# Performance work log

Measured on AMD Instinct MI355X. Metric: run time of the kernel, lower is better.

## Reference

```python
import jax, jax.numpy as jnp
import numpy as np

NUM_HEADS = 16
HEAD_DIM = 64
SCALE = HEAD_DIM ** (-0.5)


def setup_inputs() -> dict:
    key = jax.random.key(0)
    ks = jax.random.split(key, 7)
    B, T, S, D = 8, 1024, 1500, 1024
    std = 1.0 / np.sqrt(D)
    return {
        "x": jax.random.normal(ks[0], (B, T, D), jnp.float32),
        "k": jax.random.normal(ks[1], (B, S, D), jnp.float32),
        "v": jax.random.normal(ks[2], (B, S, D), jnp.float32),
        "wq": jax.random.normal(ks[3], (D, D), jnp.float32) * std,
        "bq": jnp.zeros((D,), jnp.float32),
        "wo": jax.random.normal(ks[4], (D, D), jnp.float32) * std,
        "bo": jnp.zeros((D,), jnp.float32),
    }


def reference(x, k, v, wq, bq, wo, bo):
    B, T, D = x.shape
    H, Dh = NUM_HEADS, HEAD_DIM
    # q_proj (torch Linear: x @ W^T + b), pre-scaled
    q = (jnp.einsum("btd,ed->bte", x, wq) + bq) * SCALE
    q = q.reshape(B, T, H, Dh)                      # bthd
    kh = k.reshape(B, -1, H, Dh)                    # bshd
    vh = v.reshape(B, -1, H, Dh)
    scores = jnp.einsum("bthd,bshd->bhts", q, kh)   # full [B,H,T,S]
    probs = jax.nn.softmax(scores, axis=-1)
    out = jnp.einsum("bhts,bshd->bthd", probs, vh).reshape(B, T, D)
    return jnp.einsum("btd,ed->bte", out, wo) + bo
```

## Files before the change

kernel.cpp:

```cpp
#include <hip/hip_runtime.h>
#include <hip/hip_bf16.h>

typedef __attribute__((ext_vector_type(8))) short short8;
typedef __attribute__((ext_vector_type(4))) float floatx4;

#define B_ 8
#define T_ 1024
#define S_ 1500
#define SP 1536
#define D_ 1024
#define H_ 16
#define DH 64
#define SCALE2_ 0.1803368801111244f

__device__ __forceinline__ unsigned short f2bf(float f) {
  unsigned u = __float_as_uint(f);
  u += 0x7fffu + ((u >> 16) & 1u);
  return (unsigned short)(u >> 16);
}

__device__ __forceinline__ floatx4 mfma16(short8 a, short8 b, floatx4 c) {
  return __builtin_amdgcn_mfma_f32_16x16x32_bf16(a, b, c, 0, 0, 0);
}

__device__ __forceinline__ void gload_lds16(const unsigned short* g, unsigned short* l) {
  __builtin_amdgcn_global_load_lds(
      (const __attribute__((address_space(1))) unsigned int*)g,
      (__attribute__((address_space(3))) unsigned int*)(unsigned long)(uintptr_t)l, 16, 0, 0);
}

#define N1C (B_ * T_ * D_ / 4)
#define N2C (D_ * D_ / 4)
#define NB_CAST ((N1C + 2 * N2C) / 256)
#define NB_PK (B_ * H_ * SP * 16 / 256)
#define NB_PVT ((SP / 64) * B_ * H_)
__global__ void prep_kernel(const float* __restrict__ x, const float* __restrict__ k,
                            const float* __restrict__ v, const float* __restrict__ wq,
                            const float* __restrict__ wo,
                            unsigned short* __restrict__ xb,
                            unsigned short* __restrict__ wqb,
                            unsigned short* __restrict__ wob,
                            unsigned short* __restrict__ kb,
                            unsigned short* __restrict__ vt) {
  __shared__ unsigned short tile[64][72];
  int bid = blockIdx.x;
  int t = threadIdx.x;
  if (bid < NB_CAST) {
    int i = bid * 256 + t;
    const float* src;
    unsigned short* dst;
    int j;
    if (i < N1C) {
      src = x; dst = xb; j = i;
    } else if (i < N1C + N2C) {
      src = wq; dst = wqb; j = i - N1C;
    } else {
      src = wo; dst = wob; j = i - N1C - N2C;
    }
    float4 val = ((const float4*)src)[j];
    ushort4 o;
    o.x = f2bf(val.x); o.y = f2bf(val.y); o.z = f2bf(val.z); o.w = f2bf(val.w);
    ((ushort4*)dst)[j] = o;
  } else if (bid < NB_CAST + NB_PK) {
    int i = (bid - NB_CAST) * 256 + t;
    int dh4 = (i & 15) * 4;
    int j = i >> 4;
    int s = j % SP;
    int bh = j / SP;
    if (bh < B_ * H_) {
      int b = bh >> 4, h = bh & 15;
      int p = s & 31;
      int src = (s & ~31) + ((p >> 2) & 3) * 8 + ((p >> 4) & 1) * 4 + (p & 3);
      ushort4 o;
      if (src < S_) {
        float4 val = *(const float4*)(k + (((size_t)(b * S_ + src) * H_ + h) * DH) + dh4);
        o.x = f2bf(val.x); o.y = f2bf(val.y); o.z = f2bf(val.z); o.w = f2bf(val.w);
      } else {
        o = make_ushort4(0, 0, 0, 0);
      }
      *(ushort4*)(kb + ((size_t)bh * SP + s) * DH + dh4) = o;
    }
  } else {
    int q = bid - NB_CAST - NB_PK;
    int st = q % (SP / 64), bh = q / (SP / 64);
    int b = bh >> 4, h = bh & 15;
    int s0 = st * 64;
    for (int i = t; i < 1024; i += 256) {
      int sl = i >> 4, dh4 = (i & 15) * 4;
      float4 val = make_float4(0.f, 0.f, 0.f, 0.f);
      if (s0 + sl < S_)
        val = *(const float4*)(v + ((size_t)((b * S_ + s0 + sl) * H_ + h)) * DH + dh4);
      tile[dh4 + 0][sl] = f2bf(val.x);
      tile[dh4 + 1][sl] = f2bf(val.y);
      tile[dh4 + 2][sl] = f2bf(val.z);
      tile[dh4 + 3][sl] = f2bf(val.w);
    }
    __syncthreads();
    for (int i = t; i < 1024; i += 256) {
      int d = i >> 4, s4 = (i & 15) * 4;
      ushort4 o;
      o.x = tile[d][s4]; o.y = tile[d][s4 + 1]; o.z = tile[d][s4 + 2]; o.w = tile[d][s4 + 3];
      *(ushort4*)(vt + ((size_t)bh * DH + d) * SP + s0 + s4) = o;
    }
  }
}

#define BK2 64
__global__ __launch_bounds__(256, 4) void gemm_bt(const unsigned short* __restrict__ A,
                                                  const unsigned short* __restrict__ Bm,
                                                  const float* __restrict__ bias,
                                                  void* __restrict__ outp, int epi) {
  __shared__ unsigned short As[128 * BK2];
  __shared__ unsigned short Bs[128 * BK2];
  const int K = 1024;
  int t = threadIdx.x;
  int m0 = blockIdx.y * 128, n0 = blockIdx.x * 128;
  int w = t >> 6, lane = t & 63, quad = lane >> 4, l16 = lane & 15;
  int mw = (w & 1) * 64, nw = (w >> 1) * 64;

  int rloc = lane >> 3, cslot = lane & 7;
  int gch = cslot ^ rloc;
  const unsigned short* paw = A + (size_t)(m0 + w * 8 + rloc) * K + gch * 8;
  const unsigned short* pbw = Bm + (size_t)(n0 + w * 8 + rloc) * K + gch * 8;
  unsigned short* lA = &As[(w * 8) * BK2];
  unsigned short* lB = &Bs[(w * 8) * BK2];

  floatx4 acc[4][4];
#pragma unroll
  for (int i = 0; i < 4; i++)
#pragma unroll
    for (int j = 0; j < 4; j++) {
      floatx4 z = {0.f, 0.f, 0.f, 0.f};
      acc[i][j] = z;
    }

  int arow = mw + l16;
  int brow = nw + l16;
  int sl7 = l16 & 7;

  for (int kt = 0; kt < K / BK2; kt++) {
    __syncthreads();
#pragma unroll
    for (int p2 = 0; p2 < 4; p2++) {
      gload_lds16(paw + (size_t)(p2 * 32) * K + kt * BK2, lA + p2 * 32 * BK2);
      gload_lds16(pbw + (size_t)(p2 * 32) * K + kt * BK2, lB + p2 * 32 * BK2);
    }
    __syncthreads();

#pragma unroll
    for (int hf = 0; hf < 2; hf++) {
      int slot = ((hf << 2) | quad) ^ sl7;
      short8 af[4], bf[4];
#pragma unroll
      for (int mi = 0; mi < 4; mi++)
        af[mi] = *(const short8*)&As[(arow + mi * 16) * BK2 + slot * 8];
#pragma unroll
      for (int ni = 0; ni < 4; ni++)
        bf[ni] = *(const short8*)&Bs[(brow + ni * 16) * BK2 + slot * 8];
#pragma unroll
      for (int mi = 0; mi < 4; mi++)
#pragma unroll
        for (int ni = 0; ni < 4; ni++)
          acc[mi][ni] = mfma16(af[mi], bf[ni], acc[mi][ni]);
    }
  }

#pragma unroll
  for (int mi = 0; mi < 4; mi++)
#pragma unroll
    for (int ni = 0; ni < 4; ni++) {
      int row = m0 + mw + mi * 16 + quad * 4;
      int col = n0 + nw + ni * 16 + l16;
      float bcol = bias[col];
#pragma unroll
      for (int r = 0; r < 4; r++) {
        float val = acc[mi][ni][r] + bcol;
        int rr = row + r;
        if (epi == 0) {
          int b = rr >> 10, tt = rr & 1023, h = col >> 6, dh = col & 63;
          ((unsigned short*)outp)[(((size_t)(b * 16 + h) * 1024) + tt) * 64 + dh] =
              f2bf(val * SCALE2_);
        } else {
          ((float*)outp)[(size_t)rr * 1024 + col] = val;
        }
      }
    }
}

#define NT (SP / 64)
__global__ __launch_bounds__(256, 4) void attn_kernel(
    const unsigned short* __restrict__ qs, const unsigned short* __restrict__ kb,
    const unsigned short* __restrict__ vt, unsigned short* __restrict__ ob) {
  __shared__ unsigned short Ks[2][64 * 72];
  __shared__ unsigned short Vs[2][64 * 72];
  int p = blockIdx.x + (blockIdx.y << 3);
  int ttile = p >> 7, bh = p & 127;
  int b = bh >> 4, h = bh & 15;
  int t = threadIdx.x, w = t >> 6, lane = t & 63, quad = lane >> 4, l16 = lane & 15;

  const unsigned short* qp =
      qs + ((size_t)bh * T_ + ttile * 128 + w * 32 + l16) * DH + quad * 8;
  short8 qa[2][2];
  qa[0][0] = *(const short8*)(qp);
  qa[0][1] = *(const short8*)(qp + 32);
  qa[1][0] = *(const short8*)(qp + 16 * DH);
  qa[1][1] = *(const short8*)(qp + 16 * DH + 32);

  const unsigned short* kbase = kb + (size_t)bh * SP * DH;
  const unsigned short* vbase = vt + (size_t)bh * DH * SP;

  int sr = t >> 3, c8 = (t & 7) * 8;
  const unsigned short* ksp0 = kbase + (size_t)sr * DH + c8;
  const unsigned short* ksp1 = kbase + (size_t)(sr + 32) * DH + c8;
  const unsigned short* vsp0 = vbase + (size_t)sr * SP + c8;
  const unsigned short* vsp1 = vbase + (size_t)(sr + 32) * SP + c8;
  int klo0 = sr * 72 + c8, klo1 = (sr + 32) * 72 + c8;
  int vlo0 = sr * 72 + c8, vlo1 = (sr + 32) * 72 + c8;

  floatx4 o[2][4];
#pragma unroll
  for (int g = 0; g < 2; g++)
#pragma unroll
    for (int i = 0; i < 4; i++) {
      floatx4 z = {0.f, 0.f, 0.f, 0.f};
      o[g][i] = z;
    }
  float mrow[2] = {-1e30f, -1e30f};
  float lrow[2] = {0.f, 0.f};

  int4 rk0 = *(const int4*)(ksp0);
  int4 rk1 = *(const int4*)(ksp1);
  int4 rv0 = *(const int4*)(vsp0);
  int4 rv1 = *(const int4*)(vsp1);
  *(int4*)&Ks[0][klo0] = rk0;
  *(int4*)&Ks[0][klo1] = rk1;
  *(int4*)&Vs[0][vlo0] = rv0;
  *(int4*)&Vs[0][vlo1] = rv1;
  rk0 = *(const int4*)(ksp0 + (size_t)64 * DH);
  rk1 = *(const int4*)(ksp1 + (size_t)64 * DH);
  rv0 = *(const int4*)(vsp0 + 64);
  rv1 = *(const int4*)(vsp1 + 64);

  for (int n = 0; n < NT; n++) {
    int s0 = n * 64;
    int cur = n & 1;
    __syncthreads();
    if (n + 1 < NT) {
      *(int4*)&Ks[cur ^ 1][klo0] = rk0;
      *(int4*)&Ks[cur ^ 1][klo1] = rk1;
      *(int4*)&Vs[cur ^ 1][vlo0] = rv0;
      *(int4*)&Vs[cur ^ 1][vlo1] = rv1;
    }
    if (n + 2 < NT) {
      size_t so = (size_t)(s0 + 128);
      rk0 = *(const int4*)(ksp0 + so * DH);
      rk1 = *(const int4*)(ksp1 + so * DH);
      rv0 = *(const int4*)(vsp0 + so);
      rv1 = *(const int4*)(vsp1 + so);
    }

    floatx4 sc[2][4];
#pragma unroll
    for (int nb = 0; nb < 4; nb++) {
      short8 k0 = *(const short8*)&Ks[cur][(nb * 16 + l16) * 72 + quad * 8];
      short8 k1 = *(const short8*)&Ks[cur][(nb * 16 + l16) * 72 + 32 + quad * 8];
      floatx4 a = {0.f, 0.f, 0.f, 0.f};
      a = mfma16(k0, qa[0][0], a);
      a = mfma16(k1, qa[0][1], a);
      sc[0][nb] = a;
      floatx4 a2 = {0.f, 0.f, 0.f, 0.f};
      a2 = mfma16(k0, qa[1][0], a2);
      a2 = mfma16(k1, qa[1][1], a2);
      sc[1][nb] = a2;
    }
    if (s0 + 64 > S_) {
#pragma unroll
      for (int nb = 0; nb < 4; nb++)
#pragma unroll
        for (int r = 0; r < 4; r++) {
          int s_act = s0 + (nb >> 1) * 32 + quad * 8 + (nb & 1) * 4 + r;
          if (s_act >= S_) { sc[0][nb][r] = -1e30f; sc[1][nb][r] = -1e30f; }
        }
    }

#pragma unroll
    for (int g = 0; g < 2; g++) {
      float mx = -1e30f;
#pragma unroll
      for (int nb = 0; nb < 4; nb++) {
        float a0m = fmaxf(sc[g][nb][0], sc[g][nb][1]);
        float a1m = fmaxf(sc[g][nb][2], sc[g][nb][3]);
        mx = fmaxf(mx, fmaxf(a0m, a1m));
      }
      mx = fmaxf(mx, __shfl_xor(mx, 16));
      mx = fmaxf(mx, __shfl_xor(mx, 32));
      if (__any(mx > mrow[g] + 8.0f)) {
        float mnew = fmaxf(mrow[g], mx);
        float alpha = exp2f(mrow[g] - mnew);
        mrow[g] = mnew;
        lrow[g] *= alpha;
#pragma unroll
        for (int db = 0; db < 4; db++) {
          o[g][db][0] *= alpha; o[g][db][1] *= alpha;
          o[g][db][2] *= alpha; o[g][db][3] *= alpha;
        }
      }
      float m = mrow[g];
      float rs = 0.f;
#pragma unroll
      for (int nb = 0; nb < 4; nb++)
#pragma unroll
        for (int r = 0; r < 4; r++) {
          float p2 = exp2f(sc[g][nb][r] - m);
          sc[g][nb][r] = p2;
          rs += p2;
        }
      rs += __shfl_xor(rs, 16);
      rs += __shfl_xor(rs, 32);
      lrow[g] += rs;
    }

#pragma unroll
    for (int c = 0; c < 2; c++) {
      union { short8 v; __hip_bfloat162 h[4]; } pk0, pk1;
      pk0.h[0] = __float22bfloat162_rn(make_float2(sc[0][2 * c][0], sc[0][2 * c][1]));
      pk0.h[1] = __float22bfloat162_rn(make_float2(sc[0][2 * c][2], sc[0][2 * c][3]));
      pk0.h[2] = __float22bfloat162_rn(make_float2(sc[0][2 * c + 1][0], sc[0][2 * c + 1][1]));
      pk0.h[3] = __float22bfloat162_rn(make_float2(sc[0][2 * c + 1][2], sc[0][2 * c + 1][3]));
      pk1.h[0] = __float22bfloat162_rn(make_float2(sc[1][2 * c][0], sc[1][2 * c][1]));
      pk1.h[1] = __float22bfloat162_rn(make_float2(sc[1][2 * c][2], sc[1][2 * c][3]));
      pk1.h[2] = __float22bfloat162_rn(make_float2(sc[1][2 * c + 1][0], sc[1][2 * c + 1][1]));
      pk1.h[3] = __float22bfloat162_rn(make_float2(sc[1][2 * c + 1][2], sc[1][2 * c + 1][3]));
#pragma unroll
      for (int db = 0; db < 4; db++) {
        short8 vf = *(const short8*)&Vs[cur][(db * 16 + l16) * 72 + c * 32 + quad * 8];
        o[0][db] = mfma16(vf, pk0.v, o[0][db]);
        o[1][db] = mfma16(vf, pk1.v, o[1][db]);
      }
    }
  }

#pragma unroll
  for (int g = 0; g < 2; g++) {
    float inv = 1.0f / lrow[g];
    int tg = ttile * 128 + w * 32 + g * 16 + l16;
#pragma unroll
    for (int db = 0; db < 4; db++) {
      int dh = db * 16 + quad * 4;
      union { ushort4 s4; __hip_bfloat162 h[2]; } st;
      st.h[0] = __float22bfloat162_rn(make_float2(o[g][db][0] * inv, o[g][db][1] * inv));
      st.h[1] = __float22bfloat162_rn(make_float2(o[g][db][2] * inv, o[g][db][3] * inv));
      *(ushort4*)(ob + ((size_t)(b * T_ + tg) * H_ + h) * DH + dh) = st.s4;
    }
  }
}

extern "C" void kernel_launch(void* const* d_in, const int* in_sizes, int n_in,
                              void* d_out, int out_size, void* d_ws, size_t ws_size,
                              hipStream_t stream) {
  const float* x  = (const float*)d_in[0];
  const float* k  = (const float*)d_in[1];
  const float* v  = (const float*)d_in[2];
  const float* wq = (const float*)d_in[3];
  const float* bq = (const float*)d_in[4];
  const float* wo = (const float*)d_in[5];
  const float* bo = (const float*)d_in[6];
  float* out = (float*)d_out;

  char* ws = (char*)d_ws;
  unsigned short* xb  = (unsigned short*)(ws + 0);
  unsigned short* wqb = (unsigned short*)(ws + 16777216);
  unsigned short* wob = (unsigned short*)(ws + 18874368);
  unsigned short* kbp = (unsigned short*)(ws + 20971520);
  unsigned short* vtp = (unsigned short*)(ws + 46137344);
  unsigned short* qsp = (unsigned short*)(ws + 71303168);
  unsigned short* obp = (unsigned short*)(ws + 88080384);

  prep_kernel<<<NB_CAST + NB_PK + NB_PVT, 256, 0, stream>>>(x, k, v, wq, wo, xb, wqb,
                                                            wob, kbp, vtp);
  gemm_bt<<<dim3(D_ / 128, B_ * T_ / 128), 256, 0, stream>>>(xb, wqb, bq, qsp, 0);
  attn_kernel<<<dim3(T_ / 128, B_ * H_), 256, 0, stream>>>(qsp, kbp, vtp, obp);
  gemm_bt<<<dim3(D_ / 128, B_ * T_ / 128), 256, 0, stream>>>(obp, wob, bo, out, 1);
}
```

Before: 314.2 us.

## Double-buffer LDS tiles in projection GEMM and remap block order

The projection GEMM now keeps two LDS buffers and issues the global-to-LDS loads for the next K tile before running the MFMAs on the current one, with one barrier per iteration instead of two. This is meant to overlap memory latency with compute. It also remaps block indices so consecutive blocks share A rows, which should improve L2 reuse. LDS use doubles and launch bounds drop to 2 blocks per CU, which reduces occupancy. The remap hardcodes an 8x64 grid shape.

Measured after the change: 300.8 us. 4.3% less time.

```diff
diff --git a/kernel.cpp b/kernel.cpp
--- a/kernel.cpp
+++ b/kernel.cpp
@@ -106,15 +106,18 @@
 }
 
 #define BK2 64
-__global__ __launch_bounds__(256, 4) void gemm_bt(const unsigned short* __restrict__ A,
+__global__ __launch_bounds__(256, 2) void gemm_bt(const unsigned short* __restrict__ A,
                                                   const unsigned short* __restrict__ Bm,
                                                   const float* __restrict__ bias,
                                                   void* __restrict__ outp, int epi) {
-  __shared__ unsigned short As[128 * BK2];
-  __shared__ unsigned short Bs[128 * BK2];
+  __shared__ unsigned short As[2][128 * BK2];
+  __shared__ unsigned short Bs[2][128 * BK2];
   const int K = 1024;
+  const int NKT = K / BK2;
   int t = threadIdx.x;
-  int m0 = blockIdx.y * 128, n0 = blockIdx.x * 128;
+  int p = blockIdx.x + (blockIdx.y << 3);
+  int rid = (p & 7) * 64 + (p >> 3);
+  int m0 = (rid >> 3) * 128, n0 = (rid & 7) * 128;
   int w = t >> 6, lane = t & 63, quad = lane >> 4, l16 = lane & 15;
   int mw = (w & 1) * 64, nw = (w >> 1) * 64;
 
@@ -122,8 +125,7 @@
   int gch = cslot ^ rloc;
   const unsigned short* paw = A + (size_t)(m0 + w * 8 + rloc) * K + gch * 8;
   const unsigned short* pbw = Bm + (size_t)(n0 + w * 8 + rloc) * K + gch * 8;
-  unsigned short* lA = &As[(w * 8) * BK2];
-  unsigned short* lB = &Bs[(w * 8) * BK2];
+  int lofs = (w * 8) * BK2;
 
   floatx4 acc[4][4];
 #pragma unroll
@@ -138,31 +140,42 @@
   int brow = nw + l16;
   int sl7 = l16 & 7;
 
-  for (int kt = 0; kt < K / BK2; kt++) {
-    __syncthreads();
-#pragma unroll
-    for (int p2 = 0; p2 < 4; p2++) {
-      gload_lds16(paw + (size_t)(p2 * 32) * K + kt * BK2, lA + p2 * 32 * BK2);
-      gload_lds16(pbw + (size_t)(p2 * 32) * K + kt * BK2, lB + p2 * 32 * BK2);
-    }
-    __syncthreads();
-
+#pragma unroll
+  for (int p2 = 0; p2 < 4; p2++) {
+    gload_lds16(paw + (size_t)(p2 * 32) * K, &As[0][lofs + p2 * 32 * BK2]);
+    gload_lds16(pbw + (size_t)(p2 * 32) * K, &Bs[0][lofs + p2 * 32 * BK2]);
+  }
+  __syncthreads();
+
+  int cur = 0;
+  for (int kt = 0; kt < NKT; kt++) {
+    if (kt + 1 < NKT) {
+#pragma unroll
+      for (int p2 = 0; p2 < 4; p2++) {
+        gload_lds16(paw + (size_t)(p2 * 32) * K + (kt + 1) * BK2,
+                    &As[cur ^ 1][lofs + p2 * 32 * BK2]);
+        gload_lds16(pbw + (size_t)(p2 * 32) * K + (kt + 1) * BK2,
+                    &Bs[cur ^ 1][lofs + p2 * 32 * BK2]);
+      }
+    }
 #pragma unroll
     for (int hf = 0; hf < 2; hf++) {
       int slot = ((hf << 2) | quad) ^ sl7;
       short8 af[4], bf[4];
 #pragma unroll
       for (int mi = 0; mi < 4; mi++)
-        af[mi] = *(const short8*)&As[(arow + mi * 16) * BK2 + slot * 8];
+        af[mi] = *(const short8*)&As[cur][(arow + mi * 16) * BK2 + slot * 8];
 #pragma unroll
       for (int ni = 0; ni < 4; ni++)
-        bf[ni] = *(const short8*)&Bs[(brow + ni * 16) * BK2 + slot * 8];
+        bf[ni] = *(const short8*)&Bs[cur][(brow + ni * 16) * BK2 + slot * 8];
 #pragma unroll
       for (int mi = 0; mi < 4; mi++)
 #pragma unroll
         for (int ni = 0; ni < 4; ni++)
           acc[mi][ni] = mfma16(af[mi], bf[ni], acc[mi][ni]);
     }
+    __syncthreads();
+    cur ^= 1;
   }
 
 #pragma unroll
```
